# Kernel tuning notes

Hardware: AMD Instinct MI355X
Metric: run time of the kernel (lower is better)

Reference implementation:

```python
import jax, jax.numpy as jnp
import numpy as np

# dims matching init_kwargs
B, N, D = 2, 4096, 1024
H, LH = 16, 8
GH = H - LH            # global (FAVOR+) heads
DH = D // H            # 64 per-head dim
M = 256                # performer random features
W = 256                # local attention window
EPS = 1e-4


def softmax_kernel(data, proj, is_query):
    """FAVOR+ positive softmax kernel features. data: [b,h,n,d], proj: [m,d]."""
    dn = data.shape[-1] ** -0.25                       # data_normalizer
    ratio = proj.shape[0] ** -0.5
    data_dash = jnp.einsum('bhnd,md->bhnm', data * dn, proj)
    diag = jnp.sum(data ** 2, axis=-1, keepdims=True) * 0.5 * dn ** 2
    if is_query:
        stab = jnp.max(data_dash, axis=-1, keepdims=True)
    else:
        stab = jnp.max(data_dash)
    return ratio * (jnp.exp(data_dash - diag - stab) + EPS)


def linear_attention(q, k, v):
    """Non-causal performer attention. q,k: [b,h,n,m], v: [b,h,n,d]."""
    k_sum = k.sum(axis=-2)                                        # [b,h,m]
    d_inv = 1.0 / jnp.einsum('bhnm,bhm->bhn', q, k_sum)
    ctx = jnp.einsum('bhnm,bhnd->bhmd', k, v)                     # [b,h,m,d]
    return jnp.einsum('bhnm,bhmd,bhn->bhnd', q, ctx, d_inv)


def local_attention(q, k, v, w):
    """Windowed attention: each window of w queries attends to windows i-1,i,i+1."""
    b, h, n, d = q.shape
    nw = n // w
    scale = d ** -0.5
    qw = q.reshape(b, h, nw, w, d)
    kw = k.reshape(b, h, nw, w, d)
    vw = v.reshape(b, h, nw, w, d)
    kp = jnp.pad(kw, ((0, 0), (0, 0), (1, 1), (0, 0), (0, 0)))
    vp = jnp.pad(vw, ((0, 0), (0, 0), (1, 1), (0, 0), (0, 0)))
    kk = jnp.concatenate([kp[:, :, :-2], kp[:, :, 1:-1], kp[:, :, 2:]], axis=3)  # [b,h,nw,3w,d]
    vv = jnp.concatenate([vp[:, :, :-2], vp[:, :, 1:-1], vp[:, :, 2:]], axis=3)
    wi = jnp.arange(nw)
    back_ok = jnp.broadcast_to((wi > 0)[:, None], (nw, w))
    mid_ok = jnp.ones((nw, w), dtype=bool)
    fwd_ok = jnp.broadcast_to((wi < nw - 1)[:, None], (nw, w))
    valid = jnp.concatenate([back_ok, mid_ok, fwd_ok], axis=-1)   # [nw, 3w]
    scores = jnp.einsum('bhiqd,bhikd->bhiqk', qw, kk) * scale
    scores = jnp.where(valid[None, None, :, None, :], scores, -1e9)
    attn = jax.nn.softmax(scores, axis=-1)
    out = jnp.einsum('bhiqk,bhikd->bhiqd', attn, vv)
    return out.reshape(b, h, n, d)


def _orthogonal_projection(m, d, seed=0):
    """Gaussian orthogonal random matrix (scaling=0) as in performer FeatureMap."""
    rng = np.random.default_rng(seed)
    blocks = []
    for _ in range(m // d):
        a = rng.standard_normal((d, d))
        qmat, _ = np.linalg.qr(a)
        blocks.append(qmat.T)
    un = np.concatenate(blocks, axis=0)                # [m, d] orthonormal rows per block
    mult = np.linalg.norm(rng.standard_normal((m, d)), axis=1, keepdims=True)
    return jnp.asarray(mult * un, dtype=jnp.float32)


def setup_inputs() -> dict:
    key = jax.random.key(0)
    k1, k2, k3, k4, k5, k6 = jax.random.split(key, 6)
    s = 0.02
    return {
        'x': jax.random.normal(k1, (B, N, D), dtype=jnp.float32),
        'Wq': jax.random.normal(k2, (D, D), dtype=jnp.float32) * s,
        'Wk': jax.random.normal(k3, (D, D), dtype=jnp.float32) * s,
        'Wv': jax.random.normal(k4, (D, D), dtype=jnp.float32) * s,
        'Wo': jax.random.normal(k5, (D, D), dtype=jnp.float32) * s,
        'bo': jax.random.normal(k6, (D,), dtype=jnp.float32) * s,
        'proj': _orthogonal_projection(M, DH),
    }


def reference(x, Wq, Wk, Wv, Wo, bo, proj):
    b, n, _ = x.shape
    # qkv projections (weights stored [in,out]; no qkv bias)
    q = (x @ Wq).reshape(b, n, H, DH).transpose(0, 2, 1, 3)
    k = (x @ Wk).reshape(b, n, H, DH).transpose(0, 2, 1, 3)
    v = (x @ Wv).reshape(b, n, H, DH).transpose(0, 2, 1, 3)
    # split global / local heads
    qg, ql = q[:, :GH], q[:, GH:]
    kg, kl = k[:, :GH], k[:, GH:]
    vg, vl = v[:, :GH], v[:, GH:]
    # global FAVOR+ path
    phi_q = softmax_kernel(qg, proj, is_query=True)
    phi_k = softmax_kernel(kg, proj, is_query=False)
    out_g = linear_attention(phi_q, phi_k, vg)
    # local windowed path
    out_l = local_attention(ql, kl, vl, W)
    out = jnp.concatenate([out_g, out_l], axis=1)          # [b,H,n,DH]
    out = out.transpose(0, 2, 1, 3).reshape(b, n, H * DH)
    return out @ Wo + bo
```

## Files before the change

kernel.cpp:

```cpp
#include <hip/hip_runtime.h>
#include <hip/hip_bf16.h>

#define B_ 2
#define N_ 4096
#define D_ 1024
#define QLD_ 3072
#define H_ 16
#define GH_ 8
#define DH_ 64
#define M_ 256
#define W_ 256
#define NW_ 16
#define EPS_ 1e-4f
#define RATIO_ 0.0625f
#define R_ (B_*N_)

typedef __attribute__((ext_vector_type(8))) short short8;
typedef __attribute__((ext_vector_type(4))) short short4_;
typedef __attribute__((ext_vector_type(4))) float float4_;

__device__ __forceinline__ float b2f(unsigned short u){
  union { unsigned int i; float f; } x; x.i = ((unsigned int)u) << 16; return x.f;
}
__device__ __forceinline__ unsigned short f2b(float f){
  unsigned int u = __float_as_uint(f);
  u = u + 0x7FFFu + ((u >> 16) & 1u);
  return (unsigned short)(u >> 16);
}
__device__ __forceinline__ unsigned int encf(float x){
  unsigned int u = __float_as_uint(x);
  return (u & 0x80000000u) ? ~u : (u | 0x80000000u);
}
__device__ __forceinline__ float decf(unsigned int e){
  unsigned int u = (e & 0x80000000u) ? (e ^ 0x80000000u) : ~e;
  return __uint_as_float(u);
}
__device__ __forceinline__ void gl_lds16(const unsigned short* g, unsigned short* l){
  __builtin_amdgcn_global_load_lds((const __attribute__((address_space(1))) unsigned int*)g,
                                   (__attribute__((address_space(3))) unsigned int*)l, 16, 0, 0);
}

__global__ void init_misc(unsigned int* stab_enc){
  if (threadIdx.x == 0) *stab_enc = encf(-3.0e38f);
}

__global__ void cast_f32_bf16(const float* __restrict__ src, unsigned short* __restrict__ dst, int n8){
  int i = blockIdx.x*256 + threadIdx.x;
  if (i >= n8) return;
  const float4_* sp = (const float4_*)src + (size_t)i*2;
  float4_ a = sp[0], b = sp[1];
  short8 o;
  o[0]=(short)f2b(a[0]); o[1]=(short)f2b(a[1]); o[2]=(short)f2b(a[2]); o[3]=(short)f2b(a[3]);
  o[4]=(short)f2b(b[0]); o[5]=(short)f2b(b[1]); o[6]=(short)f2b(b[2]); o[7]=(short)f2b(b[3]);
  *((short8*)dst + i) = o;
}

__global__ void cast_proj(const float* __restrict__ proj, unsigned short* __restrict__ projb){
  int i = blockIdx.x*256 + threadIdx.x;
  if (i < M_*DH_) projb[i] = f2b(proj[i]*0.35355339059327373f);
}

__global__ void transpose_w(const float* w0, const float* w1, const float* w2, const float* w3,
                            unsigned short* t0, unsigned short* t1, unsigned short* t2, unsigned short* t3){
  const float* src; unsigned short* dst;
  switch (blockIdx.z){
    case 0: src = w0; dst = t0; break;
    case 1: src = w1; dst = t1; break;
    case 2: src = w2; dst = t2; break;
    default: src = w3; dst = t3; break;
  }
  __shared__ float tile[64][65];
  int r0 = blockIdx.x*64, c0 = blockIdx.y*64;
  for (int it = 0; it < 16; ++it){
    int idx = it*256 + threadIdx.x;
    int r = idx >> 6, c = idx & 63;
    tile[r][c] = src[(size_t)(r0 + r)*D_ + c0 + c];
  }
  __syncthreads();
  for (int it = 0; it < 16; ++it){
    int idx = it*256 + threadIdx.x;
    int r = idx >> 6, c = idx & 63;
    dst[(size_t)(c0 + r)*D_ + r0 + c] = f2b(tile[c][r]);
  }
}

__global__ void transpose_v(const unsigned short* __restrict__ Vb, unsigned short* __restrict__ Vt,
                            float* __restrict__ vcol){
  __shared__ unsigned short tile[64*72];
  int nt = blockIdx.x, h = blockIdx.y, b = blockIdx.z;
  int n0 = nt*64, col0 = h*64;
  int tid = threadIdx.x;
  int r = tid >> 2, c16 = (tid & 3)*16;
  #pragma unroll
  for (int g = 0; g < 2; ++g){
    short8 v = *(const short8*)&Vb[((size_t)b*N_ + n0 + r)*QLD_ + col0 + c16 + g*8];
    #pragma unroll
    for (int e = 0; e < 8; ++e) tile[r*72 + c16 + g*8 + e] = (unsigned short)v[e];
  }
  __syncthreads();
  if (h < GH_){
    int c = tid & 63, g = tid >> 6;
    float s = 0.f;
    #pragma unroll
    for (int i = 0; i < 16; ++i) s += b2f(tile[(g*16 + i)*72 + c]);
    atomicAdd(&vcol[(b*GH_ + h)*64 + c], s);
  }
  int d = tid >> 2, ng = (tid & 3)*16;
  short8 o0, o1;
  #pragma unroll
  for (int e = 0; e < 8; ++e){ o0[e] = (short)tile[(ng + e)*72 + d]; o1[e] = (short)tile[(ng + 8 + e)*72 + d]; }
  size_t ob = ((size_t)(b*H_ + h)*64 + d)*N_ + n0 + ng;
  *(short8*)&Vt[ob] = o0;
  *(short8*)&Vt[ob + 8] = o1;
}

template<int FINAL>
__launch_bounds__(256)
__global__ void gemm_bf16(const unsigned short* __restrict__ A, const unsigned short* __restrict__ Bt,
                          unsigned short* __restrict__ Cb, float* __restrict__ Cf,
                          const float* __restrict__ bias, int K, int Ncols){
  __shared__ __attribute__((aligned(16))) unsigned short As[128*32];
  __shared__ __attribute__((aligned(16))) unsigned short Bs[128*32];
  int tid = threadIdx.x, lane = tid & 63, wave = tid >> 6;
  int bm = blockIdx.x*128, bn = blockIdx.y*128;
  int wm = (wave >> 1)*64, wn = (wave & 1)*64;
  float4_ acc[4][4];
  #pragma unroll
  for (int i = 0; i < 4; ++i)
    #pragma unroll
    for (int j = 0; j < 4; ++j)
      #pragma unroll
      for (int r = 0; r < 4; ++r) acc[i][j][r] = 0.f;
  int srow = tid >> 2, c = tid & 3;
  int scol = (c ^ ((srow >> 1) & 3))*8;
  const unsigned short* a0 = &A[(size_t)(bm + srow)*K + scol];
  const unsigned short* a1 = &A[(size_t)(bm + 64 + srow)*K + scol];
  const unsigned short* b0 = &Bt[(size_t)(bn + srow)*K + scol];
  const unsigned short* b1 = &Bt[(size_t)(bn + 64 + srow)*K + scol];
  unsigned short* la0 = &As[tid*8];
  unsigned short* la1 = &As[2048 + tid*8];
  unsigned short* lb0 = &Bs[tid*8];
  unsigned short* lb1 = &Bs[2048 + tid*8];
  int p4 = lane >> 4, l15 = lane & 15;
  for (int k0 = 0; k0 < K; k0 += 32){
    gl_lds16(a0, la0); gl_lds16(a1, la1);
    gl_lds16(b0, lb0); gl_lds16(b1, lb1);
    a0 += 32; a1 += 32; b0 += 32; b1 += 32;
    __syncthreads();
    short8 af[4], bf[4];
    #pragma unroll
    for (int i = 0; i < 4; ++i){
      int row = wm + i*16 + l15;
      af[i] = *(const short8*)&As[row*32 + (p4 ^ ((row >> 1) & 3))*8];
    }
    #pragma unroll
    for (int j = 0; j < 4; ++j){
      int row = wn + j*16 + l15;
      bf[j] = *(const short8*)&Bs[row*32 + (p4 ^ ((row >> 1) & 3))*8];
    }
    #pragma unroll
    for (int i = 0; i < 4; ++i)
      #pragma unroll
      for (int j = 0; j < 4; ++j)
        acc[i][j] = __builtin_amdgcn_mfma_f32_16x16x32_bf16(af[i], bf[j], acc[i][j], 0, 0, 0);
    __syncthreads();
  }
  int rr = p4*4, cc = l15;
  #pragma unroll
  for (int i = 0; i < 4; ++i)
    #pragma unroll
    for (int j = 0; j < 4; ++j)
      #pragma unroll
      for (int r = 0; r < 4; ++r){
        size_t row = bm + wm + i*16 + rr + r;
        int col = bn + wn + j*16 + cc;
        if (FINAL) Cf[row*(size_t)Ncols + col] = acc[i][j][r] + bias[col];
        else       Cb[row*(size_t)Ncols + col] = f2b(acc[i][j][r]);
      }
}

__launch_bounds__(256)
__global__ void phik_finish(const unsigned short* __restrict__ Kb, const unsigned short* __restrict__ projb,
                            unsigned short* __restrict__ phikT, float* __restrict__ ksum,
                            unsigned int* __restrict__ stab_enc){
  __shared__ __attribute__((aligned(16))) unsigned short pl[256*64];
  int tid = threadIdx.x, lane = tid & 63, wave = tid >> 6;
  int h = blockIdx.y, b = blockIdx.z, nb = blockIdx.x;
  int n0 = nb*64;
  int col0 = h*64;
  int kk = (lane >> 4)*8, l15 = lane & 15;
  int bh = b*GH_ + h;
  size_t rowbase = (size_t)b*N_ + n0 + wave*16;
  short8 qa[2];
  #pragma unroll
  for (int ks = 0; ks < 2; ++ks)
    qa[ks] = *(const short8*)&Kb[(rowbase + l15)*QLD_ + col0 + ks*32 + kk];
  float s = 0.f;
  #pragma unroll
  for (int ks = 0; ks < 2; ++ks)
    #pragma unroll
    for (int j = 0; j < 8; ++j){ float q = b2f((unsigned short)qa[ks][j]); s += q*q; }
  s += __shfl_xor(s, 16, 64);
  s += __shfl_xor(s, 32, 64);
  s *= 0.0625f;
  float dg[4];
  #pragma unroll
  for (int r = 0; r < 4; ++r) dg[r] = __shfl(s, (lane & 48) | ((lane >> 4)*4 + r), 64);
  float mxall = -3e38f;
  #pragma unroll
  for (int mt = 0; mt < 16; ++mt){
    float4_ a; a[0]=a[1]=a[2]=a[3]=0.f;
    #pragma unroll
    for (int ks = 0; ks < 2; ++ks){
      short8 bfr = *(const short8*)&projb[(size_t)(mt*16 + l15)*DH_ + ks*32 + kk];
      a = __builtin_amdgcn_mfma_f32_16x16x32_bf16(qa[ks], bfr, a, 0, 0, 0);
    }
    int m = mt*16 + l15;
    #pragma unroll
    for (int r = 0; r < 4; ++r){
      float ddv = a[r];
      mxall = fmaxf(mxall, ddv);
      float v = __expf(ddv - dg[r]);
      int n = wave*16 + (lane>>4)*4 + r;
      int slot = (n >> 3) ^ (m & 7);
      pl[m*64 + slot*8 + (n & 7)] = f2b(v);
    }
  }
  #pragma unroll
  for (int mm = 1; mm < 64; mm <<= 1) mxall = fmaxf(mxall, __shfl_xor(mxall, mm, 64));
  if (lane == 0) atomicMax(stab_enc, encf(mxall));
  __syncthreads();
  int m = tid;
  float ssum = 0.f;
  size_t outbase = (((size_t)bh*64 + nb)*256 + m)*64;
  #pragma unroll
  for (int j = 0; j < 8; ++j){
    int slot = j ^ (m & 7);
    short8 v = *(const short8*)&pl[m*64 + slot*8];
    #pragma unroll
    for (int e = 0; e < 8; ++e) ssum += b2f((unsigned short)v[e]);
    *(short8*)&phikT[outbase + j*8] = v;
  }
  atomicAdd(&ksum[bh*M_ + m], ssum);
}

__launch_bounds__(256)
__global__ void ctx_kernel(const unsigned short* __restrict__ phikT, const unsigned short* __restrict__ Vt,
                           float* __restrict__ ctxp){
  int tid = threadIdx.x, lane = tid & 63, wave = tid >> 6;
  int split = blockIdx.x, h = blockIdx.y, b = blockIdx.z;
  int bh = b*GH_ + h;
  int kk = (lane >> 4)*8, l15 = lane & 15;
  float4_ acc[4][4];
  #pragma unroll
  for (int i = 0; i < 4; ++i)
    #pragma unroll
    for (int j = 0; j < 4; ++j)
      #pragma unroll
      for (int r = 0; r < 4; ++r) acc[i][j][r] = 0.f;
  const unsigned short* Abase = phikT + (size_t)bh*64*256*64;
  const unsigned short* Bbase = Vt + (size_t)(b*H_ + h)*64*N_;
  int n0 = split*256;
  #pragma unroll
  for (int ks = 0; ks < 8; ++ks){
    int n = n0 + ks*32;
    int nb = n >> 6, in0 = n & 32;
    short8 af[4], bf[4];
    #pragma unroll
    for (int mt = 0; mt < 4; ++mt)
      af[mt] = *(const short8*)&Abase[((size_t)nb*256 + wave*64 + mt*16 + l15)*64 + in0 + kk];
    #pragma unroll
    for (int dt = 0; dt < 4; ++dt)
      bf[dt] = *(const short8*)&Bbase[(size_t)(dt*16 + l15)*N_ + n + kk];
    #pragma unroll
    for (int mt = 0; mt < 4; ++mt)
      #pragma unroll
      for (int dt = 0; dt < 4; ++dt)
        acc[mt][dt] = __builtin_amdgcn_mfma_f32_16x16x32_bf16(af[mt], bf[dt], acc[mt][dt], 0, 0, 0);
  }
  int rr = (lane >> 4)*4;
  float* obase = ctxp + (((size_t)split*16 + bh)*256)*64;
  #pragma unroll
  for (int mt = 0; mt < 4; ++mt)
    #pragma unroll
    for (int dt = 0; dt < 4; ++dt)
      #pragma unroll
      for (int r = 0; r < 4; ++r)
        obase[(size_t)(wave*64 + mt*16 + rr + r)*64 + dt*16 + l15] = acc[mt][dt][r];
}

__launch_bounds__(256)
__global__ void ctx_reduce(const float* __restrict__ ctxp, const float* __restrict__ vcol,
                           const unsigned int* __restrict__ stab_enc, unsigned short* __restrict__ ctxbT){
  __shared__ float tile[16*65];
  int mt = blockIdx.x, bh = blockIdx.y;
  int tid = threadIdx.x;
  float es = RATIO_*__expf(-decf(*stab_enc));
  float epsr = RATIO_*EPS_;
  int ml = tid >> 4, d4 = (tid & 15)*4;
  const float* base = ctxp + ((size_t)bh*256 + mt*16 + ml)*64 + d4;
  float4_ acc; acc[0]=acc[1]=acc[2]=acc[3]=0.f;
  #pragma unroll
  for (int sp = 0; sp < 16; ++sp){
    float4_ v = *(const float4_*)(base + (size_t)sp*16*256*64);
    acc[0] += v[0]; acc[1] += v[1]; acc[2] += v[2]; acc[3] += v[3];
  }
  #pragma unroll
  for (int e = 0; e < 4; ++e) acc[e] = es*acc[e] + epsr*vcol[bh*64 + d4 + e];
  *(float4_*)&tile[ml*65 + d4] = acc;
  __syncthreads();
  int d = tid >> 2, mg = (tid & 3)*4;
  short4_ o;
  #pragma unroll
  for (int e = 0; e < 4; ++e) o[e] = (short)f2b(tile[(mg + e)*65 + d]);
  *(short4_*)&ctxbT[((size_t)bh*64 + d)*256 + mt*16 + mg] = o;
}

__launch_bounds__(256)
__global__ void phiq_outg(const unsigned short* __restrict__ Qb, const unsigned short* __restrict__ projb,
                          const unsigned short* __restrict__ ctxbT, const float* __restrict__ ksum_u,
                          const unsigned int* __restrict__ stab_enc, unsigned short* __restrict__ attnb){
  __shared__ __attribute__((aligned(16))) unsigned short pl[4][16*256];
  __shared__ float ks_l[256];
  int tid = threadIdx.x, lane = tid & 63, wave = tid >> 6;
  int h = blockIdx.y, b = blockIdx.z;
  int n0 = blockIdx.x*64;
  int col0 = h*64;
  int bh = b*GH_ + h;
  int p4 = lane >> 4, l15 = lane & 15, kk = p4*8;
  {
    float es = __expf(-decf(*stab_enc));
    ks_l[tid] = RATIO_*(es*ksum_u[bh*M_ + tid] + EPS_*(float)N_);
  }
  __syncthreads();
  size_t rowbase = (size_t)b*N_ + n0 + wave*16;
  short8 qa[2];
  #pragma unroll
  for (int ks = 0; ks < 2; ++ks)
    qa[ks] = *(const short8*)&Qb[(rowbase + l15)*QLD_ + col0 + ks*32 + kk];
  float s = 0.f;
  #pragma unroll
  for (int ks = 0; ks < 2; ++ks)
    #pragma unroll
    for (int j = 0; j < 8; ++j){ float q = b2f((unsigned short)qa[ks][j]); s += q*q; }
  s += __shfl_xor(s, 16, 64);
  s += __shfl_xor(s, 32, 64);
  s *= 0.0625f;
  float dg[4];
  #pragma unroll
  for (int r = 0; r < 4; ++r) dg[r] = __shfl(s, (lane & 48) | (p4*4 + r), 64);
  float4_ dd[16];
  #pragma unroll
  for (int mt = 0; mt < 16; ++mt){
    float4_ a; a[0]=a[1]=a[2]=a[3]=0.f;
    #pragma unroll
    for (int ks = 0; ks < 2; ++ks){
      short8 bfr = *(const short8*)&projb[(size_t)(mt*16 + l15)*DH_ + ks*32 + kk];
      a = __builtin_amdgcn_mfma_f32_16x16x32_bf16(qa[ks], bfr, a, 0, 0, 0);
    }
    dd[mt] = a;
  }
  unsigned short* plw = &pl[wave][0];
  float dinv[4];
  #pragma unroll
  for (int r = 0; r < 4; ++r){
    float mx = dd[0][r];
    #pragma unroll
    for (int mt = 1; mt < 16; ++mt) mx = fmaxf(mx, dd[mt][r]);
    mx = fmaxf(mx, __shfl_xor(mx, 1, 64));
    mx = fmaxf(mx, __shfl_xor(mx, 2, 64));
    mx = fmaxf(mx, __shfl_xor(mx, 4, 64));
    mx = fmaxf(mx, __shfl_xor(mx, 8, 64));
    float sb = mx + dg[r];
    int row = p4*4 + r;
    float dpr = 0.f;
    #pragma unroll
    for (int mt = 0; mt < 16; ++mt){
      float v = RATIO_*(__expf(dd[mt][r] - sb) + EPS_);
      dpr += v*ks_l[mt*16 + l15];
      int q = mt*2 + (l15 >> 3);
      plw[row*256 + ((q ^ (row & 7)) << 3) + (l15 & 7)] = f2b(v);
    }
    dpr += __shfl_xor(dpr, 1, 64);
    dpr += __shfl_xor(dpr, 2, 64);
    dpr += __shfl_xor(dpr, 4, 64);
    dpr += __shfl_xor(dpr, 8, 64);
    dinv[r] = 1.f/dpr;
  }
  float4_ acc[4];
  #pragma unroll
  for (int dt = 0; dt < 4; ++dt){ acc[dt][0]=acc[dt][1]=acc[dt][2]=acc[dt][3]=0.f; }
  #pragma unroll
  for (int ks = 0; ks < 8; ++ks){
    int q = ks*4 + p4;
    short8 af = *(const short8*)&plw[l15*256 + ((q ^ (l15 & 7)) << 3)];
    #pragma unroll
    for (int dt = 0; dt < 4; ++dt){
      short8 bf = *(const short8*)&ctxbT[((size_t)bh*64 + dt*16 + l15)*M_ + ks*32 + kk];
      acc[dt] = __builtin_amdgcn_mfma_f32_16x16x32_bf16(af, bf, acc[dt], 0, 0, 0);
    }
  }
  #pragma unroll
  for (int dt = 0; dt < 4; ++dt)
    #pragma unroll
    for (int r = 0; r < 4; ++r){
      int rloc = wave*16 + p4*4 + r;
      attnb[((size_t)b*N_ + n0 + rloc)*D_ + col0 + dt*16 + l15] = f2b(acc[dt][r]*dinv[r]);
    }
}

__launch_bounds__(256)
__global__ void local_attn_kernel(const unsigned short* __restrict__ Qb, const unsigned short* __restrict__ Kb,
                                  const unsigned short* __restrict__ Vt, unsigned short* __restrict__ attnb){
  int tid = threadIdx.x, lane = tid & 63, wv = tid >> 6;
  int bx = blockIdx.x, hl = blockIdx.y, b = blockIdx.z;
  int w = bx >> 1;
  int col0 = (GH_ + hl)*64;
  int q0 = bx*128 + wv*32;
  int l15 = lane & 15, p4 = lane >> 4, kk = p4*8;
  int sA = ((l15 >> 2) << 3) + (l15 & 3);
  const unsigned short* Kbase = Kb + (size_t)b*N_*QLD_ + col0;
  const unsigned short* Vrow  = Vt + (size_t)(b*H_ + GH_ + hl)*64*N_;
  short8 qa[2][2];
  #pragma unroll
  for (int qt = 0; qt < 2; ++qt)
    #pragma unroll
    for (int ks = 0; ks < 2; ++ks){
      short8 v = *(const short8*)&Qb[((size_t)b*N_ + q0 + qt*16 + l15)*QLD_ + col0 + ks*32 + kk];
      #pragma unroll
      for (int j = 0; j < 8; ++j) v[j] = (short)f2b(b2f((unsigned short)v[j])*0.125f);
      qa[qt][ks] = v;
    }
  float l_part[2] = {0.f, 0.f};
  float4_ accv[2][4];
  #pragma unroll
  for (int qt = 0; qt < 2; ++qt)
    #pragma unroll
    for (int dt = 0; dt < 4; ++dt){ accv[qt][dt][0]=accv[qt][dt][1]=accv[qt][dt][2]=accv[qt][dt][3]=0.f; }
  int wlo = (w > 0) ? w - 1 : 0;
  int whi = (w < NW_ - 1) ? w + 1 : NW_ - 1;
  for (int wi = wlo; wi <= whi; ++wi){
    #pragma unroll
    for (int c = 0; c < 4; ++c){
      int key0 = wi*W_ + c*64;
      const unsigned short* Kc = Kbase + (size_t)key0*QLD_;
      float4_ s[2][4];
      #pragma unroll
      for (int qt = 0; qt < 2; ++qt)
        #pragma unroll
        for (int kt = 0; kt < 4; ++kt){ s[qt][kt][0]=s[qt][kt][1]=s[qt][kt][2]=s[qt][kt][3]=0.f; }
      #pragma unroll
      for (int ks = 0; ks < 2; ++ks){
        short8 kb0 = *(const short8*)&Kc[(size_t)(sA +  0)*QLD_ + ks*32 + kk];
        short8 kb1 = *(const short8*)&Kc[(size_t)(sA +  4)*QLD_ + ks*32 + kk];
        short8 kb2 = *(const short8*)&Kc[(size_t)(sA + 32)*QLD_ + ks*32 + kk];
        short8 kb3 = *(const short8*)&Kc[(size_t)(sA + 36)*QLD_ + ks*32 + kk];
        #pragma unroll
        for (int qt = 0; qt < 2; ++qt){
          s[qt][0] = __builtin_amdgcn_mfma_f32_16x16x32_bf16(kb0, qa[qt][ks], s[qt][0], 0, 0, 0);
          s[qt][1] = __builtin_amdgcn_mfma_f32_16x16x32_bf16(kb1, qa[qt][ks], s[qt][1], 0, 0, 0);
          s[qt][2] = __builtin_amdgcn_mfma_f32_16x16x32_bf16(kb2, qa[qt][ks], s[qt][2], 0, 0, 0);
          s[qt][3] = __builtin_amdgcn_mfma_f32_16x16x32_bf16(kb3, qa[qt][ks], s[qt][3], 0, 0, 0);
        }
      }
      short8 af[2][2];
      #pragma unroll
      for (int qt = 0; qt < 2; ++qt){
        float p[4][4];
        float rs = 0.f;
        #pragma unroll
        for (int kt = 0; kt < 4; ++kt)
          #pragma unroll
          for (int r = 0; r < 4; ++r){
            p[kt][r] = __expf(s[qt][kt][r]);
            rs += p[kt][r];
          }
        l_part[qt] += rs;
        #pragma unroll
        for (int half = 0; half < 2; ++half){
          short8 a;
          #pragma unroll
          for (int r = 0; r < 4; ++r){
            a[r]     = (short)f2b(p[half*2 + 0][r]);
            a[r + 4] = (short)f2b(p[half*2 + 1][r]);
          }
          af[qt][half] = a;
        }
      }
      #pragma unroll
      for (int ks = 0; ks < 2; ++ks){
        short8 vb0 = *(const short8*)&Vrow[(size_t)( 0 + l15)*N_ + key0 + ks*32 + kk];
        short8 vb1 = *(const short8*)&Vrow[(size_t)(16 + l15)*N_ + key0 + ks*32 + kk];
        short8 vb2 = *(const short8*)&Vrow[(size_t)(32 + l15)*N_ + key0 + ks*32 + kk];
        short8 vb3 = *(const short8*)&Vrow[(size_t)(48 + l15)*N_ + key0 + ks*32 + kk];
        #pragma unroll
        for (int qt = 0; qt < 2; ++qt){
          accv[qt][0] = __builtin_amdgcn_mfma_f32_16x16x32_bf16(af[qt][ks], vb0, accv[qt][0], 0, 0, 0);
          accv[qt][1] = __builtin_amdgcn_mfma_f32_16x16x32_bf16(af[qt][ks], vb1, accv[qt][1], 0, 0, 0);
          accv[qt][2] = __builtin_amdgcn_mfma_f32_16x16x32_bf16(af[qt][ks], vb2, accv[qt][2], 0, 0, 0);
          accv[qt][3] = __builtin_amdgcn_mfma_f32_16x16x32_bf16(af[qt][ks], vb3, accv[qt][3], 0, 0, 0);
        }
      }
    }
  }
  #pragma unroll
  for (int qt = 0; qt < 2; ++qt){
    float lv = l_part[qt];
    lv += __shfl_xor(lv, 16, 64);
    lv += __shfl_xor(lv, 32, 64);
    float ilq[4];
    #pragma unroll
    for (int r = 0; r < 4; ++r)
      ilq[r] = 1.f/__shfl(lv, (lane & 48) | (p4*4 + r), 64);
    #pragma unroll
    for (int dt = 0; dt < 4; ++dt)
      #pragma unroll
      for (int r = 0; r < 4; ++r)
        attnb[((size_t)b*N_ + q0 + qt*16 + p4*4 + r)*D_ + col0 + dt*16 + l15] = f2b(accv[qt][dt][r]*ilq[r]);
  }
}

extern "C" void kernel_launch(void* const* d_in, const int* in_sizes, int n_in,
                              void* d_out, int out_size, void* d_ws, size_t ws_size,
                              hipStream_t stream){
  const float* x    = (const float*)d_in[0];
  const float* Wq   = (const float*)d_in[1];
  const float* Wk   = (const float*)d_in[2];
  const float* Wv   = (const float*)d_in[3];
  const float* Wo   = (const float*)d_in[4];
  const float* bo   = (const float*)d_in[5];
  const float* proj = (const float*)d_in[6];
  float* out = (float*)d_out;
  char* ws = (char*)d_ws;

  const size_t o_Wqt  = 0;
  const size_t o_Wkt  = o_Wqt  + (size_t)D_*D_*2;
  const size_t o_Wvt  = o_Wkt  + (size_t)D_*D_*2;
  const size_t o_Wot  = o_Wvt  + (size_t)D_*D_*2;
  const size_t o_Xb   = o_Wot  + (size_t)D_*D_*2;
  const size_t o_QKV  = o_Xb   + (size_t)R_*D_*2;
  const size_t o_Vt   = o_QKV  + (size_t)R_*QLD_*2;
  const size_t o_phikT= o_Vt   + (size_t)B_*H_*DH_*N_*2;
  const size_t o_ctxp = o_phikT+ (size_t)B_*GH_*N_*M_*2;
  const size_t o_ksum = o_ctxp + (size_t)16*B_*GH_*M_*DH_*4;
  const size_t o_vcol = o_ksum + (size_t)B_*GH_*M_*4;
  const size_t o_ctxT = o_vcol + (size_t)B_*GH_*DH_*4;
  const size_t o_projb= o_ctxT + (size_t)B_*GH_*DH_*M_*2;
  const size_t o_stab = o_projb+ (size_t)M_*DH_*2;

  unsigned short* Wqt  = (unsigned short*)(ws + o_Wqt);
  unsigned short* Wkt  = (unsigned short*)(ws + o_Wkt);
  unsigned short* Wvt  = (unsigned short*)(ws + o_Wvt);
  unsigned short* Wot  = (unsigned short*)(ws + o_Wot);
  unsigned short* Xb   = (unsigned short*)(ws + o_Xb);
  unsigned short* attnb= Xb;
  unsigned short* QKV  = (unsigned short*)(ws + o_QKV);
  unsigned short* Vt   = (unsigned short*)(ws + o_Vt);
  unsigned short* phikT= (unsigned short*)(ws + o_phikT);
  float*          ctxp = (float*)(ws + o_ctxp);
  float*          ksum = (float*)(ws + o_ksum);
  float*          vcol = (float*)(ws + o_vcol);
  unsigned short* ctxT = (unsigned short*)(ws + o_ctxT);
  unsigned short* projb= (unsigned short*)(ws + o_projb);
  unsigned int*   stab = (unsigned int*)(ws + o_stab);

  (void)in_sizes; (void)n_in; (void)out_size; (void)ws_size;

  (void)hipMemsetAsync(ws + o_ksum, 0, (size_t)B_*GH_*M_*4 + (size_t)B_*GH_*DH_*4, stream);
  init_misc<<<1, 1, 0, stream>>>(stab);
  cast_f32_bf16<<<R_*D_/8/256, 256, 0, stream>>>(x, Xb, R_*D_/8);
  cast_proj<<<64, 256, 0, stream>>>(proj, projb);
  transpose_w<<<dim3(16,16,4), 256, 0, stream>>>(Wq, Wk, Wv, Wo, Wqt, Wkt, Wvt, Wot);

  gemm_bf16<0><<<dim3(64,24), 256, 0, stream>>>(Xb, Wqt, QKV, nullptr, nullptr, D_, QLD_);

  transpose_v<<<dim3(64,16,2), 256, 0, stream>>>(QKV + 2048, Vt, vcol);

  phik_finish<<<dim3(64,8,2), 256, 0, stream>>>(QKV + 1024, projb, phikT, ksum, stab);

  ctx_kernel<<<dim3(16,8,2), 256, 0, stream>>>(phikT, Vt, ctxp);
  ctx_reduce<<<dim3(16,16), 256, 0, stream>>>(ctxp, vcol, stab, ctxT);
  phiq_outg<<<dim3(64,8,2), 256, 0, stream>>>(QKV, projb, ctxT, ksum, stab, attnb);
  local_attn_kernel<<<dim3(32,8,2), 256, 0, stream>>>(QKV, QKV + 1024, Vt, attnb);

  gemm_bf16<1><<<dim3(64,8), 256, 0, stream>>>(attnb, Wot, nullptr, out, bo, D_, D_);
}
```

Before: 299.9 us.

## Fuse phi_k feature computation with context accumulation via LDS and atomics

The phi_k kernel now keeps the bf16 feature tile in shared memory and multiplies it directly against V to accumulate the context matrix with float atomicAdd. This removes the phikT global round-trip (about 16 MB written and re-read), the per-split ctxp partial buffers and the reduction pass. The init kernel is folded into cast_proj, and the local attention grid is remapped so each XCD handles contiguous head/batch pairs. In exchange there are many fp32 atomics into a small context buffer (64 blocks per head) and a non-deterministic summation order.

New measurement: 318.6 us. 1.06x slower.

```diff
diff --git a/kernel.cpp b/kernel.cpp
--- a/kernel.cpp
+++ b/kernel.cpp
@@ -40,10 +40,6 @@
                                    (__attribute__((address_space(3))) unsigned int*)l, 16, 0, 0);
 }
 
-__global__ void init_misc(unsigned int* stab_enc){
-  if (threadIdx.x == 0) *stab_enc = encf(-3.0e38f);
-}
-
 __global__ void cast_f32_bf16(const float* __restrict__ src, unsigned short* __restrict__ dst, int n8){
   int i = blockIdx.x*256 + threadIdx.x;
   if (i >= n8) return;
@@ -55,8 +51,10 @@
   *((short8*)dst + i) = o;
 }
 
-__global__ void cast_proj(const float* __restrict__ proj, unsigned short* __restrict__ projb){
+__global__ void cast_proj(const float* __restrict__ proj, unsigned short* __restrict__ projb,
+                          unsigned int* __restrict__ stab_enc){
   int i = blockIdx.x*256 + threadIdx.x;
+  if (i == 0) *stab_enc = encf(-3.0e38f);
   if (i < M_*DH_) projb[i] = f2b(proj[i]*0.35355339059327373f);
 }
 
@@ -180,15 +178,15 @@
 }
 
 __launch_bounds__(256)
-__global__ void phik_finish(const unsigned short* __restrict__ Kb, const unsigned short* __restrict__ projb,
-                            unsigned short* __restrict__ phikT, float* __restrict__ ksum,
-                            unsigned int* __restrict__ stab_enc){
+__global__ void phik_ctx(const unsigned short* __restrict__ Kb, const unsigned short* __restrict__ projb,
+                         const unsigned short* __restrict__ Vt, float* __restrict__ ctx,
+                         float* __restrict__ ksum, unsigned int* __restrict__ stab_enc){
   __shared__ __attribute__((aligned(16))) unsigned short pl[256*64];
   int tid = threadIdx.x, lane = tid & 63, wave = tid >> 6;
   int h = blockIdx.y, b = blockIdx.z, nb = blockIdx.x;
   int n0 = nb*64;
   int col0 = h*64;
-  int kk = (lane >> 4)*8, l15 = lane & 15;
+  int p4 = lane >> 4, l15 = lane & 15, kk = p4*8;
   int bh = b*GH_ + h;
   size_t rowbase = (size_t)b*N_ + n0 + wave*16;
   short8 qa[2];
@@ -205,7 +203,7 @@
   s *= 0.0625f;
   float dg[4];
   #pragma unroll
-  for (int r = 0; r < 4; ++r) dg[r] = __shfl(s, (lane & 48) | ((lane >> 4)*4 + r), 64);
+  for (int r = 0; r < 4; ++r) dg[r] = __shfl(s, (lane & 48) | (p4*4 + r), 64);
   float mxall = -3e38f;
   #pragma unroll
   for (int mt = 0; mt < 16; ++mt){
@@ -221,7 +219,7 @@
       float ddv = a[r];
       mxall = fmaxf(mxall, ddv);
       float v = __expf(ddv - dg[r]);
-      int n = wave*16 + (lane>>4)*4 + r;
+      int n = wave*16 + p4*4 + r;
       int slot = (n >> 3) ^ (m & 7);
       pl[m*64 + slot*8 + (n & 7)] = f2b(v);
     }
@@ -230,27 +228,18 @@
   for (int mm = 1; mm < 64; mm <<= 1) mxall = fmaxf(mxall, __shfl_xor(mxall, mm, 64));
   if (lane == 0) atomicMax(stab_enc, encf(mxall));
   __syncthreads();
-  int m = tid;
-  float ssum = 0.f;
-  size_t outbase = (((size_t)bh*64 + nb)*256 + m)*64;
-  #pragma unroll
-  for (int j = 0; j < 8; ++j){
-    int slot = j ^ (m & 7);
-    short8 v = *(const short8*)&pl[m*64 + slot*8];
-    #pragma unroll
-    for (int e = 0; e < 8; ++e) ssum += b2f((unsigned short)v[e]);
-    *(short8*)&phikT[outbase + j*8] = v;
-  }
-  atomicAdd(&ksum[bh*M_ + m], ssum);
-}
-
-__launch_bounds__(256)
-__global__ void ctx_kernel(const unsigned short* __restrict__ phikT, const unsigned short* __restrict__ Vt,
-                           float* __restrict__ ctxp){
-  int tid = threadIdx.x, lane = tid & 63, wave = tid >> 6;
-  int split = blockIdx.x, h = blockIdx.y, b = blockIdx.z;
-  int bh = b*GH_ + h;
-  int kk = (lane >> 4)*8, l15 = lane & 15;
+  {
+    int m = tid;
+    float ssum = 0.f;
+    #pragma unroll
+    for (int j = 0; j < 8; ++j){
+      int slot = j ^ (m & 7);
+      short8 v = *(const short8*)&pl[m*64 + slot*8];
+      #pragma unroll
+      for (int e = 0; e < 8; ++e) ssum += b2f((unsigned short)v[e]);
+    }
+    atomicAdd(&ksum[bh*M_ + m], ssum);
+  }
   float4_ acc[4][4];
   #pragma unroll
   for (int i = 0; i < 4; ++i)
@@ -258,55 +247,48 @@
     for (int j = 0; j < 4; ++j)
       #pragma unroll
       for (int r = 0; r < 4; ++r) acc[i][j][r] = 0.f;
-  const unsigned short* Abase = phikT + (size_t)bh*64*256*64;
   const unsigned short* Bbase = Vt + (size_t)(b*H_ + h)*64*N_;
-  int n0 = split*256;
-  #pragma unroll
-  for (int ks = 0; ks < 8; ++ks){
-    int n = n0 + ks*32;
-    int nb = n >> 6, in0 = n & 32;
+  #pragma unroll
+  for (int ks = 0; ks < 2; ++ks){
     short8 af[4], bf[4];
     #pragma unroll
-    for (int mt = 0; mt < 4; ++mt)
-      af[mt] = *(const short8*)&Abase[((size_t)nb*256 + wave*64 + mt*16 + l15)*64 + in0 + kk];
+    for (int mt = 0; mt < 4; ++mt){
+      int m = wave*64 + mt*16 + l15;
+      int q = ks*4 + p4;
+      af[mt] = *(const short8*)&pl[m*64 + (q ^ (m & 7))*8];
+    }
     #pragma unroll
     for (int dt = 0; dt < 4; ++dt)
-      bf[dt] = *(const short8*)&Bbase[(size_t)(dt*16 + l15)*N_ + n + kk];
+      bf[dt] = *(const short8*)&Bbase[(size_t)(dt*16 + l15)*N_ + n0 + ks*32 + kk];
     #pragma unroll
     for (int mt = 0; mt < 4; ++mt)
       #pragma unroll
       for (int dt = 0; dt < 4; ++dt)
         acc[mt][dt] = __builtin_amdgcn_mfma_f32_16x16x32_bf16(af[mt], bf[dt], acc[mt][dt], 0, 0, 0);
   }
-  int rr = (lane >> 4)*4;
-  float* obase = ctxp + (((size_t)split*16 + bh)*256)*64;
+  int rr = p4*4;
   #pragma unroll
   for (int mt = 0; mt < 4; ++mt)
     #pragma unroll
     for (int dt = 0; dt < 4; ++dt)
       #pragma unroll
       for (int r = 0; r < 4; ++r)
-        obase[(size_t)(wave*64 + mt*16 + rr + r)*64 + dt*16 + l15] = acc[mt][dt][r];
+        atomicAdd(&ctx[((size_t)bh*M_ + wave*64 + mt*16 + rr + r)*64 + dt*16 + l15], acc[mt][dt][r]);
 }
 
 __launch_bounds__(256)
-__global__ void ctx_reduce(const float* __restrict__ ctxp, const float* __restrict__ vcol,
-                           const unsigned int* __restrict__ stab_enc, unsigned short* __restrict__ ctxbT){
+__global__ void ctx_finalize(const float* __restrict__ ctx, const float* __restrict__ vcol,
+                             const unsigned int* __restrict__ stab_enc, unsigned short* __restrict__ ctxbT){
   __shared__ float tile[16*65];
   int mt = blockIdx.x, bh = blockIdx.y;
   int tid = threadIdx.x;
   float es = RATIO_*__expf(-decf(*stab_enc));
   float epsr = RATIO_*EPS_;
   int ml = tid >> 4, d4 = (tid & 15)*4;
-  const float* base = ctxp + ((size_t)bh*256 + mt*16 + ml)*64 + d4;
-  float4_ acc; acc[0]=acc[1]=acc[2]=acc[3]=0.f;
-  #pragma unroll
-  for (int sp = 0; sp < 16; ++sp){
-    float4_ v = *(const float4_*)(base + (size_t)sp*16*256*64);
-    acc[0] += v[0]; acc[1] += v[1]; acc[2] += v[2]; acc[3] += v[3];
-  }
-  #pragma unroll
-  for (int e = 0; e < 4; ++e) acc[e] = es*acc[e] + epsr*vcol[bh*64 + d4 + e];
+  float4_ v = *(const float4_*)&ctx[((size_t)bh*M_ + mt*16 + ml)*64 + d4];
+  float4_ acc;
+  #pragma unroll
+  for (int e = 0; e < 4; ++e) acc[e] = es*v[e] + epsr*vcol[bh*64 + d4 + e];
   *(float4_*)&tile[ml*65 + d4] = acc;
   __syncthreads();
   int d = tid >> 2, mg = (tid & 3)*4;
@@ -413,7 +395,11 @@
 __global__ void local_attn_kernel(const unsigned short* __restrict__ Qb, const unsigned short* __restrict__ Kb,
                                   const unsigned short* __restrict__ Vt, unsigned short* __restrict__ attnb){
   int tid = threadIdx.x, lane = tid & 63, wv = tid >> 6;
-  int bx = blockIdx.x, hl = blockIdx.y, b = blockIdx.z;
+  int wg = blockIdx.x;
+  int xcd = wg & 7, k = wg >> 3;
+  int pair = xcd*2 + (k >> 5);
+  int bx = k & 31;
+  int hl = pair & 7, b = pair >> 3;
   int w = bx >> 1;
   int col0 = (GH_ + hl)*64;
   int q0 = bx*128 + wv*32;
@@ -540,11 +526,10 @@
   const size_t o_Xb   = o_Wot  + (size_t)D_*D_*2;
   const size_t o_QKV  = o_Xb   + (size_t)R_*D_*2;
   const size_t o_Vt   = o_QKV  + (size_t)R_*QLD_*2;
-  const size_t o_phikT= o_Vt   + (size_t)B_*H_*DH_*N_*2;
-  const size_t o_ctxp = o_phikT+ (size_t)B_*GH_*N_*M_*2;
-  const size_t o_ksum = o_ctxp + (size_t)16*B_*GH_*M_*DH_*4;
+  const size_t o_ksum = o_Vt   + (size_t)B_*H_*DH_*N_*2;
   const size_t o_vcol = o_ksum + (size_t)B_*GH_*M_*4;
-  const size_t o_ctxT = o_vcol + (size_t)B_*GH_*DH_*4;
+  const size_t o_ctx  = o_vcol + (size_t)B_*GH_*DH_*4;
+  const size_t o_ctxT = o_ctx  + (size_t)B_*GH_*M_*DH_*4;
   const size_t o_projb= o_ctxT + (size_t)B_*GH_*DH_*M_*2;
   const size_t o_stab = o_projb+ (size_t)M_*DH_*2;
 
@@ -556,32 +541,29 @@
   unsigned short* attnb= Xb;
   unsigned short* QKV  = (unsigned short*)(ws + o_QKV);
   unsigned short* Vt   = (unsigned short*)(ws + o_Vt);
-  unsigned short* phikT= (unsigned short*)(ws + o_phikT);
-  float*          ctxp = (float*)(ws + o_ctxp);
   float*          ksum = (float*)(ws + o_ksum);
   float*          vcol = (float*)(ws + o_vcol);
+  float*          ctx  = (float*)(ws + o_ctx);
   unsigned short* ctxT = (unsigned short*)(ws + o_ctxT);
   unsigned short* projb= (unsigned short*)(ws + o_projb);
   unsigned int*   stab = (unsigned int*)(ws + o_stab);
 
   (void)in_sizes; (void)n_in; (void)out_size; (void)ws_size;
 
-  (void)hipMemsetAsync(ws + o_ksum, 0, (size_t)B_*GH_*M_*4 + (size_t)B_*GH_*DH_*4, stream);
-  init_misc<<<1, 1, 0, stream>>>(stab);
+  (void)hipMemsetAsync(ws + o_ksum, 0,
+                       (size_t)B_*GH_*M_*4 + (size_t)B_*GH_*DH_*4 + (size_t)B_*GH_*M_*DH_*4, stream);
   cast_f32_bf16<<<R_*D_/8/256, 256, 0, stream>>>(x, Xb, R_*D_/8);
-  cast_proj<<<64, 256, 0, stream>>>(proj, projb);
+  cast_proj<<<64, 256, 0, stream>>>(proj, projb, stab);
   transpose_w<<<dim3(16,16,4), 256, 0, stream>>>(Wq, Wk, Wv, Wo, Wqt, Wkt, Wvt, Wot);
 
   gemm_bf16<0><<<dim3(64,24), 256, 0, stream>>>(Xb, Wqt, QKV, nullptr, nullptr, D_, QLD_);
 
   transpose_v<<<dim3(64,16,2), 256, 0, stream>>>(QKV + 2048, Vt, vcol);
 
-  phik_finish<<<dim3(64,8,2), 256, 0, stream>>>(QKV + 1024, projb, phikT, ksum, stab);
-
-  ctx_kernel<<<dim3(16,8,2), 256, 0, stream>>>(phikT, Vt, ctxp);
-  ctx_reduce<<<dim3(16,16), 256, 0, stream>>>(ctxp, vcol, stab, ctxT);
+  phik_ctx<<<dim3(64,8,2), 256, 0, stream>>>(QKV + 1024, projb, Vt, ctx, ksum, stab);
+  ctx_finalize<<<dim3(16,16), 256, 0, stream>>>(ctx, vcol, stab, ctxT);
   phiq_outg<<<dim3(64,8,2), 256, 0, stream>>>(QKV, projb, ctxT, ksum, stab, attnb);
-  local_attn_kernel<<<dim3(32,8,2), 256, 0, stream>>>(QKV, QKV + 1024, Vt, attnb);
+  local_attn_kernel<<<512, 256, 0, stream>>>(QKV, QKV + 1024, Vt, attnb);
 
   gemm_bf16<1><<<dim3(64,8), 256, 0, stream>>>(attnb, Wot, nullptr, out, bo, D_, D_);
 }
```
